# Optimization experiments

Hardware: AMD Instinct MI355X
Metric: run time of the kernel (lower is better)

## Reference

```python
import jax, jax.numpy as jnp
import numpy as np

DIM = 256
NUM_HEADS = 4
HEAD_DIM = DIM // NUM_HEADS
SCALE = HEAD_DIM ** -0.5


def setup_inputs() -> dict:
    key = jax.random.key(0)
    ks = jax.random.split(key, 11)
    B, Nq, Nkv = 4, 2048, 2048
    inp = {
        "query_feat": jax.random.normal(ks[0], (B, Nq, DIM), dtype=jnp.float32),
        "key_value_feat": jax.random.normal(ks[1], (B, Nkv, DIM), dtype=jnp.float32),
        "reliability_kv": jax.random.uniform(ks[2], (B, Nkv), dtype=jnp.float32),
        "Wq": jax.random.normal(ks[3], (DIM, DIM), dtype=jnp.float32) * (DIM ** -0.5),
        "bq": jnp.zeros((DIM,), jnp.float32),
        "Wk": jax.random.normal(ks[4], (DIM, DIM), dtype=jnp.float32) * (DIM ** -0.5),
        "bk": jnp.zeros((DIM,), jnp.float32),
        "Wv": jax.random.normal(ks[5], (DIM, DIM), dtype=jnp.float32) * (DIM ** -0.5),
        "bv": jnp.zeros((DIM,), jnp.float32),
        "Wo": jax.random.normal(ks[6], (DIM, DIM), dtype=jnp.float32) * (DIM ** -0.5),
        "bo": jnp.zeros((DIM,), jnp.float32),
    }
    return inp


def _heads(x):
    B, N, C = x.shape
    return x.reshape(B, N, NUM_HEADS, HEAD_DIM).transpose(0, 2, 1, 3)  # [B,H,N,hd]


def reference(query_feat, key_value_feat, reliability_kv, Wq, bq, Wk, bk, Wv, bv, Wo, bo):
    B, Nq, _ = query_feat.shape
    q = _heads(query_feat @ Wq + bq)          # [B,H,Nq,hd]
    k = _heads(key_value_feat @ Wk + bk)      # [B,H,Nkv,hd]
    v = _heads(key_value_feat @ Wv + bv)
    # gate K/V by reliability (broadcast over heads and head_dim)
    rk = reliability_kv[:, None, :, None]     # [B,1,Nkv,1]
    k = k * rk
    v = v * rk
    attn = jnp.einsum("bhqd,bhkd->bhqk", q, k) * SCALE
    log_r = jnp.log(jnp.clip(reliability_kv, 1e-6))[:, None, None, :]  # [B,1,1,Nkv]
    attn = jax.nn.softmax(attn + log_r, axis=-1)  # [B,H,Nq,Nkv]
    out = jnp.einsum("bhqk,bhkd->bhqd", attn, v)
    out = out.transpose(0, 2, 1, 3).reshape(B, Nq, DIM)
    out = out @ Wo + bo
    attn_mean = attn.mean(axis=1)  # [B,Nq,Nkv]
    return out, attn_mean
```

## Files before the change

### kernel.cpp

```cpp
#include <hip/hip_runtime.h>


typedef __attribute__((ext_vector_type(8))) _Float16 half8;
typedef __attribute__((ext_vector_type(4))) _Float16 half4;
typedef __attribute__((ext_vector_type(2))) __fp16 fp16x2;
typedef __attribute__((ext_vector_type(4))) float f32x4;

#define MFMAH32(A, B, C) __builtin_amdgcn_mfma_f32_16x16x32_f16((A), (B), (C), 0, 0, 0)
#define MFMAH16(A, B, C) __builtin_amdgcn_mfma_f32_16x16x16f16((A), (B), (C), 0, 0, 0)

__device__ __forceinline__ unsigned short f2h(float f) {
    union { _Float16 h; unsigned short u; } c; c.h = (_Float16)f; return c.u;
}
__device__ __forceinline__ float h2f(unsigned short u) {
    union { unsigned short u; _Float16 h; } c; c.u = u; return (float)c.h;
}
__device__ __forceinline__ half8 ldh8(const unsigned short* p) {
    return *reinterpret_cast<const half8*>(p);
}
__device__ __forceinline__ half4 ldh4(const unsigned short* p) {
    return *reinterpret_cast<const half4*>(p);
}
__device__ __forceinline__ half4 pk4(float a, float b, float c, float d) {
    union { fp16x2 h2[2]; half4 h4; } u;
    u.h2[0] = __builtin_amdgcn_cvt_pkrtz(a, b);
    u.h2[1] = __builtin_amdgcn_cvt_pkrtz(c, d);
    return u.h4;
}
__device__ __forceinline__ void gld16(const unsigned short* g, unsigned short* l) {
    __builtin_amdgcn_global_load_lds(
        (const __attribute__((address_space(1))) unsigned int*)g,
        (__attribute__((address_space(3))) unsigned int*)l, 16, 0, 0);
}

__global__ void wsplit_kernel(const float* __restrict__ Wq, const float* __restrict__ Wk,
                              const float* __restrict__ Wv, const float* __restrict__ Wo,
                              unsigned short* __restrict__ WT) {
    int e = blockIdx.x * 256 + threadIdx.x;
    int m = e >> 16;
    int idx = e & 65535;
    int k = idx >> 8, n = idx & 255;
    const float* W = (m == 0) ? Wq : (m == 1) ? Wk : (m == 2) ? Wv : Wo;
    WT[m * 65536 + n * 256 + k] = f2h(W[idx]);
}

#define STAGE_W(dst_, src_, kt_) do {                                               \
    _Pragma("unroll")                                                               \
    for (int j_ = 0; j_ < 4; ++j_) {                                                \
        int s_ = w * 4 + j_;                                                        \
        int rowl_ = 8 * s_ + (l >> 3);                                              \
        int so_ = rowl_ * 256 + (kt_) * 64 + (((l & 7) ^ (rowl_ & 7)) << 3);        \
        gld16(&(src_)[so_], &(dst_)[s_ * 512]);                                     \
    }                                                                               \
} while (0)

#define GEMM_TILE(buf_, kt_) do {                                                   \
    _Pragma("unroll")                                                               \
    for (int ksl_ = 0; ksl_ < 2; ++ksl_) {                                          \
        _Pragma("unroll")                                                           \
        for (int n_ = 0; n_ < 16; ++n_) {                                           \
            int r_ = n_ * 16 + l15;                                                 \
            int idx_ = r_ * 64 + ((((ksl_)*4 + lg) ^ (r_ & 7)) << 3);               \
            half8 b_ = ldh8(&(buf_)[idx_]);                                         \
            acc[n_] = MFMAH32(ah[(kt_) * 2 + ksl_], b_, acc[n_]);                   \
        }                                                                           \
    }                                                                               \
} while (0)

__global__ __launch_bounds__(512, 1) void proj3_kernel(
    const float* __restrict__ query, const float* __restrict__ kv,
    const float* __restrict__ rel, const unsigned short* __restrict__ WT,
    const float* __restrict__ bq, const float* __restrict__ bk, const float* __restrict__ bv,
    unsigned short* __restrict__ Qh, unsigned short* __restrict__ Kh,
    unsigned short* __restrict__ Vtmp) {
    const int job = blockIdx.y;
    const float* X = (job == 0) ? query : kv;
    const unsigned short* wg = WT + job * 65536;
    const float* bias = (job == 0) ? bq : (job == 1) ? bk : bv;
    const float* rs = (job == 0) ? nullptr : rel;
    unsigned short* oh = (job == 0) ? Qh : (job == 1) ? Kh : Vtmp;

    __shared__ __align__(16) unsigned short wlds[2][256 * 64];

    const int w = threadIdx.x >> 6, l = threadIdx.x & 63;
    const int l15 = l & 15, lg = l >> 4;
    const int arow = blockIdx.x * 128 + w * 16 + l15;

    half8 ah[8];
#pragma unroll
    for (int ks = 0; ks < 8; ++ks) {
        const float* p = &X[arow * 256 + ks * 32 + lg * 8];
        float4 f0 = *reinterpret_cast<const float4*>(p);
        float4 f1 = *reinterpret_cast<const float4*>(p + 4);
        half8 t;
        t[0] = (_Float16)f0.x; t[1] = (_Float16)f0.y; t[2] = (_Float16)f0.z; t[3] = (_Float16)f0.w;
        t[4] = (_Float16)f1.x; t[5] = (_Float16)f1.y; t[6] = (_Float16)f1.z; t[7] = (_Float16)f1.w;
        ah[ks] = t;
    }
    f32x4 acc[16];
#pragma unroll
    for (int n = 0; n < 16; ++n) acc[n] = (f32x4){0.f, 0.f, 0.f, 0.f};

    STAGE_W(wlds[0], wg, 0);
    __syncthreads();
#pragma unroll
    for (int kt = 0; kt < 4; ++kt) {
        const int cur = kt & 1, nx = cur ^ 1;
        if (kt < 3) STAGE_W(wlds[nx], wg, kt + 1);
        GEMM_TILE(wlds[cur], kt);
        __syncthreads();
    }

    const int orow0 = blockIdx.x * 128 + w * 16 + lg * 4;
    float rsv[4];
#pragma unroll
    for (int r = 0; r < 4; ++r) rsv[r] = rs ? rs[orow0 + r] : 1.0f;
#pragma unroll
    for (int n = 0; n < 16; ++n) {
        const int col = n * 16 + l15;
        const float bn = bias[col];
#pragma unroll
        for (int r = 0; r < 4; ++r)
            oh[(orow0 + r) * 256 + col] = f2h((acc[n][r] + bn) * rsv[r]);
    }
}

__global__ void transpose_v_kernel(const unsigned short* __restrict__ Vtmp,
                                   unsigned short* __restrict__ Vt) {
    __shared__ unsigned short tile[16][264];
    const int st = blockIdx.x, b = blockIdx.y;
    const int t = threadIdx.x;
#pragma unroll
    for (int it = 0; it < 4; ++it) {
        int idx = it * 256 + t;
        int kr = idx >> 6;
        int d4 = (idx & 63) * 4;
        ushort4 v = *reinterpret_cast<const ushort4*>(
            &Vtmp[(size_t)(b * 2048 + st * 16 + kr) * 256 + d4]);
        tile[kr][d4 + 0] = v.x; tile[kr][d4 + 1] = v.y;
        tile[kr][d4 + 2] = v.z; tile[kr][d4 + 3] = v.w;
    }
    __syncthreads();
    {
        const int d = t;
        unsigned int u[8];
#pragma unroll
        for (int k2 = 0; k2 < 8; ++k2)
            u[k2] = (unsigned int)tile[k2 * 2][d] | ((unsigned int)tile[k2 * 2 + 1][d] << 16);
        uint4* dst = reinterpret_cast<uint4*>(&Vt[((size_t)(b * 128 + st) * 256 + d) * 16]);
        dst[0] = (uint4){u[0], u[1], u[2], u[3]};
        dst[1] = (uint4){u[4], u[5], u[6], u[7]};
    }
}

__global__ __launch_bounds__(512, 2) void attn_pass1(
    const unsigned short* __restrict__ Qh, const unsigned short* __restrict__ Kh,
    const unsigned short* __restrict__ Vt, const float* __restrict__ rel,
    float* __restrict__ po_a, float* __restrict__ po_b, float* __restrict__ ps) {
    const int bid = blockIdx.x;
    const int sw = (bid & 7) * 32 + (bid >> 3);
    const int b = sw >> 6;
    const int rem = sw & 63;
    const int kh = rem & 1;
    const int q0 = (rem >> 1) * 64;
    const int tid = threadIdx.x;
    const int w = tid >> 6, h = w & 3, ks = w >> 2;
    const int l = tid & 63, l15 = l & 15, lg = l >> 4;
    const float C2 = 0.18033688011112042f;

    __shared__ __align__(16) unsigned short ldsKV[2][8][2][1024];
    __shared__ float rel_lr[2048];
    __shared__ float ssum_sh[2][4][64];

    {
        float4 v = reinterpret_cast<const float4*>(&rel[b * 2048])[tid];
        float* d = &rel_lr[tid * 4];
        d[0] = log2f(fmaxf(v.x, 1e-6f)); d[1] = log2f(fmaxf(v.y, 1e-6f));
        d[2] = log2f(fmaxf(v.z, 1e-6f)); d[3] = log2f(fmaxf(v.w, 1e-6f));
    }

    half8 qf[4][2];
#pragma unroll
    for (int qs = 0; qs < 4; ++qs)
#pragma unroll
        for (int kd = 0; kd < 2; ++kd)
            qf[qs][kd] = ldh8(&Qh[(b * 2048 + q0 + qs * 16 + l15) * 256 +
                                  h * 64 + kd * 32 + lg * 8]);
    __syncthreads();

    const int st0 = kh * 64 + ks * 32;

#define STG(buf_, i_) do {                                                          \
    const unsigned short* kbp_ = Kh + (size_t)(b * 2048 + (st0 + (i_)) * 16) * 256  \
                                 + h * 64;                                          \
    _Pragma("unroll")                                                               \
    for (int j_ = 0; j_ < 2; ++j_) {                                                \
        int r_ = j_ * 8 + (l >> 3);                                                 \
        gld16(kbp_ + r_ * 256 + (((l & 7) ^ ((l >> 3) & 7)) << 3),                  \
              &ldsKV[0][w][buf_][j_ * 512]);                                        \
    }                                                                               \
    const unsigned short* vbp_ = Vt + (size_t)((b * 128 + st0 + (i_)) * 256         \
                                 + h * 64) * 16;                                    \
    _Pragma("unroll")                                                               \
    for (int j_ = 0; j_ < 2; ++j_) {                                                \
        int d_ = j_ * 32 + (l >> 1);                                                \
        gld16(vbp_ + d_ * 16 + (((l & 1) ^ ((l >> 1) & 1)) << 3),                   \
              &ldsKV[1][w][buf_][j_ * 512]);                                        \
    }                                                                               \
} while (0)

    float ssum[4] = {0.f, 0.f, 0.f, 0.f};
    f32x4 oacc[4][4];
#pragma unroll
    for (int qs = 0; qs < 4; ++qs)
#pragma unroll
        for (int dc = 0; dc < 4; ++dc)
            oacc[qs][dc] = (f32x4){0.f, 0.f, 0.f, 0.f};

    STG(0, 0);
    for (int i = 0; i < 32; ++i) {
        const int cur = i & 1, nx = cur ^ 1;
        if (i < 31) {
            STG(nx, i + 1);
            asm volatile("s_waitcnt vmcnt(4)" ::: "memory");
        } else {
            asm volatile("s_waitcnt vmcnt(0)" ::: "memory");
        }
        __builtin_amdgcn_sched_barrier(0);
        half8 kf0 = ldh8(&ldsKV[0][w][cur][l15 * 64 + ((lg ^ (l15 & 7)) << 3)]);
        half8 kf1 = ldh8(&ldsKV[0][w][cur][l15 * 64 + (((4 + lg) ^ (l15 & 7)) << 3)]);
        f32x4 a[4];
#pragma unroll
        for (int qs = 0; qs < 4; ++qs) {
            f32x4 t = (f32x4){0.f, 0.f, 0.f, 0.f};
            t = MFMAH32(kf0, qf[qs][0], t);
            t = MFMAH32(kf1, qf[qs][1], t);
            a[qs] = t;
        }
        float4 lr4 = *reinterpret_cast<const float4*>(&rel_lr[(st0 + i) * 16 + lg * 4]);
        half4 pa[4];
#pragma unroll
        for (int qs = 0; qs < 4; ++qs) {
            float p0 = exp2f(__builtin_fmaf(a[qs][0], C2, lr4.x));
            float p1 = exp2f(__builtin_fmaf(a[qs][1], C2, lr4.y));
            float p2 = exp2f(__builtin_fmaf(a[qs][2], C2, lr4.z));
            float p3 = exp2f(__builtin_fmaf(a[qs][3], C2, lr4.w));
            ssum[qs] += (p0 + p1) + (p2 + p3);
            pa[qs] = pk4(p0, p1, p2, p3);
        }
#pragma unroll
        for (int dc = 0; dc < 4; ++dc) {
            const int d = dc * 16 + l15;
            half4 vf = ldh4(&ldsKV[1][w][cur][d * 16 +
                            ((((lg >> 1) ^ (d & 1))) << 3) + (lg & 1) * 4]);
#pragma unroll
            for (int qs = 0; qs < 4; ++qs)
                oacc[qs][dc] = MFMAH16(pa[qs], vf, oacc[qs][dc]);
        }
    }
#undef STG

    float vred[4];
#pragma unroll
    for (int qs = 0; qs < 4; ++qs) {
        float v = ssum[qs];
        v += __shfl_xor(v, 16); v += __shfl_xor(v, 32);
        vred[qs] = v;
    }

    __syncthreads();
    if (l < 16) {
#pragma unroll
        for (int qs = 0; qs < 4; ++qs)
            ssum_sh[ks][h][qs * 16 + l] = vred[qs];
    }
    float* obuf = (float*)&ldsKV[0][0][0][0];
    if (ks == 1) {
#pragma unroll
        for (int qs = 0; qs < 4; ++qs)
#pragma unroll
            for (int dc = 0; dc < 4; ++dc)
#pragma unroll
                for (int r = 0; r < 4; ++r)
                    obuf[(qs * 16 + lg * 4 + r) * 256 + h * 64 + dc * 16 + l15] =
                        oacc[qs][dc][r];
    }
    __syncthreads();
    if (ks == 0) {
        const int chunk = b * 2 + kh;
        float* po = (chunk < 2) ? (po_a + (size_t)chunk * 524288)
                                : (po_b + (size_t)(chunk - 2) * 524288);
#pragma unroll
        for (int qs = 0; qs < 4; ++qs)
#pragma unroll
            for (int dc = 0; dc < 4; ++dc)
#pragma unroll
                for (int r = 0; r < 4; ++r) {
                    const int d = h * 64 + dc * 16 + l15;
                    const int q = qs * 16 + lg * 4 + r;
                    po[(size_t)(q0 + q) * 256 + d] = oacc[qs][dc][r] + obuf[q * 256 + d];
                }
        if (l < 16) {
#pragma unroll
            for (int qs = 0; qs < 4; ++qs)
                ps[(chunk * 4 + h) * 2048 + q0 + qs * 16 + l] =
                    ssum_sh[0][h][qs * 16 + l] + ssum_sh[1][h][qs * 16 + l];
        }
    }
}

__global__ __launch_bounds__(256) void combine_kernel(
    const float* __restrict__ po_a, const float* __restrict__ po_b,
    const float* __restrict__ ps, unsigned short* __restrict__ AO,
    float* __restrict__ sinv_ws) {
    const int t = blockIdx.x * 256 + threadIdx.x;
    const int d4 = t & 63;
    const int bq = t >> 6;
    const int q = bq & 2047;
    const int b = bq >> 11;
    const int d0 = d4 * 4, h = d0 >> 6;
    const int c0 = b * 2, c1 = b * 2 + 1;
    const float* p0 = (c0 < 2) ? po_a + (size_t)c0 * 524288 : po_b + (size_t)(c0 - 2) * 524288;
    const float* p1 = (c1 < 2) ? po_a + (size_t)c1 * 524288 : po_b + (size_t)(c1 - 2) * 524288;
    float4 x = *reinterpret_cast<const float4*>(&p0[(size_t)q * 256 + d0]);
    float4 y = *reinterpret_cast<const float4*>(&p1[(size_t)q * 256 + d0]);
    float s = ps[(c0 * 4 + h) * 2048 + q] + ps[(c1 * 4 + h) * 2048 + q];
    float si = 1.0f / s;
    ushort4 o;
    o.x = f2h((x.x + y.x) * si); o.y = f2h((x.y + y.y) * si);
    o.z = f2h((x.z + y.z) * si); o.w = f2h((x.w + y.w) * si);
    *reinterpret_cast<ushort4*>(&AO[((size_t)(b * 2048 + q)) * 256 + d0]) = o;
    if (d4 == (h << 4)) sinv_ws[(b * 4 + h) * 2048 + q] = si;
}

__global__ __launch_bounds__(256, 4) void attn_mean_kernel(
    const unsigned short* __restrict__ Qh, const unsigned short* __restrict__ Kh,
    const float* __restrict__ rel, const float* __restrict__ sinv_ws,
    float* __restrict__ attn_mean) {
    const int kslice = blockIdx.x >> 7;
    const int inner = blockIdx.x & 127;
    const int sw = (inner & 7) * 16 + (inner >> 3);
    const int b = sw >> 5;
    const int q0 = (sw & 31) * 64;
    const int tid = threadIdx.x;
    const int w = tid >> 6;
    const int l = tid & 63, l15 = l & 15, lg = l >> 4;
    const int kb = b * 2048;
    const float C2 = 0.18033688011112042f;

    __shared__ __align__(16) unsigned short ldsK[2][8192];
    __shared__ float rel_lr[2048];

#define STAGE_KM(dst_, kt_) do {                                                    \
    _Pragma("unroll")                                                               \
    for (int j_ = 0; j_ < 4; ++j_) {                                                \
        int s_ = w * 4 + j_;                                                        \
        int r_ = 2 * s_ + (l >> 5);                                                 \
        size_t so_ = (size_t)(kb + (kt_) * 32 + r_) * 256 +                         \
                     (((l & 31) ^ (r_ & 7)) << 3);                                  \
        gld16(&Kh[so_], &(dst_)[s_ * 512]);                                         \
    }                                                                               \
} while (0)

    {
        float4 v0 = reinterpret_cast<const float4*>(&rel[b * 2048])[tid * 2];
        float4 v1 = reinterpret_cast<const float4*>(&rel[b * 2048])[tid * 2 + 1];
        float* d = &rel_lr[tid * 8];
        d[0] = log2f(fmaxf(v0.x, 1e-6f)); d[1] = log2f(fmaxf(v0.y, 1e-6f));
        d[2] = log2f(fmaxf(v0.z, 1e-6f)); d[3] = log2f(fmaxf(v0.w, 1e-6f));
        d[4] = log2f(fmaxf(v1.x, 1e-6f)); d[5] = log2f(fmaxf(v1.y, 1e-6f));
        d[6] = log2f(fmaxf(v1.z, 1e-6f)); d[7] = log2f(fmaxf(v1.w, 1e-6f));
    }

    half8 qf[4][2];
    {
        const int qrow = b * 2048 + q0 + w * 16 + l15;
#pragma unroll
        for (int h = 0; h < 4; ++h)
#pragma unroll
            for (int kd = 0; kd < 2; ++kd)
                qf[h][kd] = ldh8(&Qh[qrow * 256 + h * 64 + kd * 32 + lg * 8]);
    }
    float lsi[4][4];
#pragma unroll
    for (int h = 0; h < 4; ++h)
#pragma unroll
        for (int r4 = 0; r4 < 4; ++r4)
            lsi[h][r4] = log2f(sinv_ws[(b * 4 + h) * 2048 + q0 + w * 16 + lg * 4 + r4]) - 2.0f;
    __syncthreads();

    const int kt0 = kslice * 8;
    STAGE_KM(ldsK[0], kt0);
    for (int ki = 0; ki < 8; ++ki) {
        const int kt = kt0 + ki;
        const int cur = ki & 1, nx = cur ^ 1;
        if (ki < 7) {
            STAGE_KM(ldsK[nx], kt + 1);
            asm volatile("s_waitcnt vmcnt(4)" ::: "memory");
        } else {
            asm volatile("s_waitcnt vmcnt(0)" ::: "memory");
        }
        asm volatile("s_barrier" ::: "memory");
        __builtin_amdgcn_sched_barrier(0);
#pragma unroll
        for (int kc = 0; kc < 2; ++kc) {
            const int r = kc * 16 + l15;
            const int rx = r & 7;
            f32x4 a[4];
#pragma unroll
            for (int h = 0; h < 4; ++h) {
                half8 kf0 = ldh8(&ldsK[cur][r * 256 + (((h * 8 + lg) ^ rx) << 3)]);
                half8 kf1 = ldh8(&ldsK[cur][r * 256 + (((h * 8 + 4 + lg) ^ rx) << 3)]);
                f32x4 t = (f32x4){0.f, 0.f, 0.f, 0.f};
                t = MFMAH32(qf[h][0], kf0, t);
                t = MFMAH32(qf[h][1], kf1, t);
                a[h] = t;
            }
            const float lr = rel_lr[kt * 32 + kc * 16 + l15];
            const size_t kcol = (size_t)(kt * 32 + kc * 16 + l15);
#pragma unroll
            for (int r4 = 0; r4 < 4; ++r4) {
                float m = exp2f(__builtin_fmaf(a[0][r4], C2, lsi[0][r4]) + lr)
                        + exp2f(__builtin_fmaf(a[1][r4], C2, lsi[1][r4]) + lr)
                        + exp2f(__builtin_fmaf(a[2][r4], C2, lsi[2][r4]) + lr)
                        + exp2f(__builtin_fmaf(a[3][r4], C2, lsi[3][r4]) + lr);
                attn_mean[(size_t)(b * 2048 + q0 + w * 16 + lg * 4 + r4) * 2048 + kcol] = m;
            }
        }
        asm volatile("s_waitcnt lgkmcnt(0)\n\ts_barrier" ::: "memory");
    }
#undef STAGE_KM
}

__global__ __launch_bounds__(512, 1) void final_kernel(
    const unsigned short* __restrict__ AO, const unsigned short* __restrict__ WoT,
    const float* __restrict__ bo, float* __restrict__ out) {
    __shared__ __align__(16) unsigned short wlds[2][256 * 64];

    const int w = threadIdx.x >> 6, l = threadIdx.x & 63;
    const int l15 = l & 15, lg = l >> 4;
    const int arow = blockIdx.x * 128 + w * 16 + l15;

    half8 ah[8];
#pragma unroll
    for (int ks = 0; ks < 8; ++ks)
        ah[ks] = ldh8(&AO[arow * 256 + ks * 32 + lg * 8]);
    f32x4 acc[16];
#pragma unroll
    for (int n = 0; n < 16; ++n) acc[n] = (f32x4){0.f, 0.f, 0.f, 0.f};

    STAGE_W(wlds[0], WoT, 0);
    __syncthreads();
#pragma unroll
    for (int kt = 0; kt < 4; ++kt) {
        const int cur = kt & 1, nx = cur ^ 1;
        if (kt < 3) STAGE_W(wlds[nx], WoT, kt + 1);
        GEMM_TILE(wlds[cur], kt);
        __syncthreads();
    }

    const int orow0 = blockIdx.x * 128 + w * 16 + lg * 4;
#pragma unroll
    for (int n = 0; n < 16; ++n) {
        const int col = n * 16 + l15;
        const float bn = bo[col];
#pragma unroll
        for (int r = 0; r < 4; ++r)
            out[(orow0 + r) * 256 + col] = acc[n][r] + bn;
    }
}

extern "C" void kernel_launch(void* const* d_in, const int* in_sizes, int n_in,
                              void* d_out, int out_size, void* d_ws, size_t ws_size,
                              hipStream_t stream) {
    const float* query = (const float*)d_in[0];
    const float* kv    = (const float*)d_in[1];
    const float* rel   = (const float*)d_in[2];
    const float* Wq    = (const float*)d_in[3];
    const float* bq    = (const float*)d_in[4];
    const float* Wk    = (const float*)d_in[5];
    const float* bk    = (const float*)d_in[6];
    const float* Wv    = (const float*)d_in[7];
    const float* bv    = (const float*)d_in[8];
    const float* Wo    = (const float*)d_in[9];
    const float* bo    = (const float*)d_in[10];

    char* ws = (char*)d_ws;
    unsigned short* WT   = (unsigned short*)(ws + 0);
    unsigned short* Qh   = (unsigned short*)(ws + 524288);
    unsigned short* Kh   = (unsigned short*)(ws + 4718592);
    unsigned short* Vtmp = (unsigned short*)(ws + 8912896);
    unsigned short* Vt   = (unsigned short*)(ws + 13107200);
    unsigned short* AO   = (unsigned short*)(ws + 17301504);
    float*          sinv = (float*)(ws + 21495808);
    float*          ps   = (float*)(ws + 21626880);
    float*          po_b = (float*)(ws + 21889024);
    float*          po_a = (float*)Vtmp;

    float* out = (float*)d_out;
    float* attn_mean = (float*)d_out + 2097152;

    wsplit_kernel<<<1024, 256, 0, stream>>>(Wq, Wk, Wv, Wo, WT);
    proj3_kernel<<<dim3(64, 3), 512, 0, stream>>>(query, kv, rel, WT,
                                                  bq, bk, bv, Qh, Kh, Vtmp);
    transpose_v_kernel<<<dim3(128, 4), 256, 0, stream>>>(Vtmp, Vt);
    attn_pass1<<<256, 512, 0, stream>>>(Qh, Kh, Vt, rel, po_a, po_b, ps);
    combine_kernel<<<2048, 256, 0, stream>>>(po_a, po_b, ps, AO, sinv);
    attn_mean_kernel<<<1024, 256, 0, stream>>>(Qh, Kh, rel, sinv, attn_mean);
    final_kernel<<<64, 512, 0, stream>>>(AO, WT + 3 * 65536, bo, out);
}
```

Measured before the change: 109.8 us.

## Re-split attention pass into smaller blocks with one q-tile per wave

The first attention pass now launches 1024 blocks of 256 threads instead of 256 blocks of 512. Each block handles 16 queries, and each wave covers one head over a full 64-tile key half. This removes the intra-block split-K reduction through LDS and its barriers, and raises the block count to fill more CUs. The cost is four times more K/V traffic per query, since each K/V tile now feeds only one 16-row query tile. Both the attention pass and the attn_mean kernel also precompute their global load base offsets once and advance them by a running offset, which cuts per-iteration address arithmetic.

```diff
diff --git a/kernel.cpp b/kernel.cpp
--- a/kernel.cpp
+++ b/kernel.cpp
@@ -153,160 +153,120 @@
     }
 }
 
-__global__ __launch_bounds__(512, 2) void attn_pass1(
+__global__ __launch_bounds__(256, 4) void attn_pass1(
     const unsigned short* __restrict__ Qh, const unsigned short* __restrict__ Kh,
     const unsigned short* __restrict__ Vt, const float* __restrict__ rel,
     float* __restrict__ po_a, float* __restrict__ po_b, float* __restrict__ ps) {
     const int bid = blockIdx.x;
-    const int sw = (bid & 7) * 32 + (bid >> 3);
-    const int b = sw >> 6;
-    const int rem = sw & 63;
+    const int sw = (bid & 7) * 128 + (bid >> 3);
+    const int b = sw >> 8;
+    const int rem = sw & 255;
     const int kh = rem & 1;
-    const int q0 = (rem >> 1) * 64;
+    const int q0 = (rem >> 1) * 16;
     const int tid = threadIdx.x;
-    const int w = tid >> 6, h = w & 3, ks = w >> 2;
+    const int w = tid >> 6, h = w;
     const int l = tid & 63, l15 = l & 15, lg = l >> 4;
     const float C2 = 0.18033688011112042f;
 
-    __shared__ __align__(16) unsigned short ldsKV[2][8][2][1024];
+    __shared__ __align__(16) unsigned short ldsKV[2][4][2][1024];
     __shared__ float rel_lr[2048];
-    __shared__ float ssum_sh[2][4][64];
-
-    {
-        float4 v = reinterpret_cast<const float4*>(&rel[b * 2048])[tid];
-        float* d = &rel_lr[tid * 4];
-        d[0] = log2f(fmaxf(v.x, 1e-6f)); d[1] = log2f(fmaxf(v.y, 1e-6f));
-        d[2] = log2f(fmaxf(v.z, 1e-6f)); d[3] = log2f(fmaxf(v.w, 1e-6f));
-    }
-
-    half8 qf[4][2];
-#pragma unroll
-    for (int qs = 0; qs < 4; ++qs)
-#pragma unroll
-        for (int kd = 0; kd < 2; ++kd)
-            qf[qs][kd] = ldh8(&Qh[(b * 2048 + q0 + qs * 16 + l15) * 256 +
-                                  h * 64 + kd * 32 + lg * 8]);
+
+    {
+        float4 v0 = reinterpret_cast<const float4*>(&rel[b * 2048])[tid * 2];
+        float4 v1 = reinterpret_cast<const float4*>(&rel[b * 2048])[tid * 2 + 1];
+        float* d = &rel_lr[tid * 8];
+        d[0] = log2f(fmaxf(v0.x, 1e-6f)); d[1] = log2f(fmaxf(v0.y, 1e-6f));
+        d[2] = log2f(fmaxf(v0.z, 1e-6f)); d[3] = log2f(fmaxf(v0.w, 1e-6f));
+        d[4] = log2f(fmaxf(v1.x, 1e-6f)); d[5] = log2f(fmaxf(v1.y, 1e-6f));
+        d[6] = log2f(fmaxf(v1.z, 1e-6f)); d[7] = log2f(fmaxf(v1.w, 1e-6f));
+    }
+
+    half8 qf0, qf1;
+    {
+        const int o0 = (b * 2048 + q0 + l15) * 256 + h * 64 + lg * 8;
+        qf0 = ldh8(&Qh[o0]); qf1 = ldh8(&Qh[o0 + 32]);
+    }
     __syncthreads();
 
-    const int st0 = kh * 64 + ks * 32;
-
-#define STG(buf_, i_) do {                                                          \
-    const unsigned short* kbp_ = Kh + (size_t)(b * 2048 + (st0 + (i_)) * 16) * 256  \
-                                 + h * 64;                                          \
-    _Pragma("unroll")                                                               \
-    for (int j_ = 0; j_ < 2; ++j_) {                                                \
-        int r_ = j_ * 8 + (l >> 3);                                                 \
-        gld16(kbp_ + r_ * 256 + (((l & 7) ^ ((l >> 3) & 7)) << 3),                  \
-              &ldsKV[0][w][buf_][j_ * 512]);                                        \
-    }                                                                               \
-    const unsigned short* vbp_ = Vt + (size_t)((b * 128 + st0 + (i_)) * 256         \
-                                 + h * 64) * 16;                                    \
-    _Pragma("unroll")                                                               \
-    for (int j_ = 0; j_ < 2; ++j_) {                                                \
-        int d_ = j_ * 32 + (l >> 1);                                                \
-        gld16(vbp_ + d_ * 16 + (((l & 1) ^ ((l >> 1) & 1)) << 3),                   \
-              &ldsKV[1][w][buf_][j_ * 512]);                                        \
-    }                                                                               \
+    const int st0 = kh * 64;
+
+    size_t kb_[2], vb_[2];
+    {
+        const int swzK = ((l & 7) ^ ((l >> 3) & 7)) << 3;
+        const int swzV = ((l & 1) ^ ((l >> 1) & 1)) << 3;
+#pragma unroll
+        for (int j = 0; j < 2; ++j) {
+            int kr = j * 8 + (l >> 3);
+            kb_[j] = (size_t)(b * 2048 + st0 * 16 + kr) * 256 + h * 64 + swzK;
+            int vd = j * 32 + (l >> 1);
+            vb_[j] = (size_t)((b * 128 + st0) * 256 + h * 64 + vd) * 16 + swzV;
+        }
+    }
+    unsigned short* myK = &ldsKV[0][w][0][0];
+    unsigned short* myV = &ldsKV[1][w][0][0];
+    const int kOff0 = l15 * 64 + ((lg ^ (l15 & 7)) << 3);
+    const int kOff1 = l15 * 64 + (((4 + lg) ^ (l15 & 7)) << 3);
+    int vOff[4];
+#pragma unroll
+    for (int dc = 0; dc < 4; ++dc)
+        vOff[dc] = (dc * 16 + l15) * 16 + (((lg >> 1) ^ (l15 & 1)) << 3) + (lg & 1) * 4;
+
+#define STG2(buf_, off_) do {                                                       \
+    gld16(&Kh[kb_[0] + (off_)], &myK[(buf_) * 1024]);                               \
+    gld16(&Kh[kb_[1] + (off_)], &myK[(buf_) * 1024 + 512]);                         \
+    gld16(&Vt[vb_[0] + (off_)], &myV[(buf_) * 1024]);                               \
+    gld16(&Vt[vb_[1] + (off_)], &myV[(buf_) * 1024 + 512]);                         \
 } while (0)
 
-    float ssum[4] = {0.f, 0.f, 0.f, 0.f};
-    f32x4 oacc[4][4];
-#pragma unroll
-    for (int qs = 0; qs < 4; ++qs)
-#pragma unroll
-        for (int dc = 0; dc < 4; ++dc)
-            oacc[qs][dc] = (f32x4){0.f, 0.f, 0.f, 0.f};
-
-    STG(0, 0);
-    for (int i = 0; i < 32; ++i) {
+    float ssum = 0.f;
+    f32x4 oacc[4];
+#pragma unroll
+    for (int dc = 0; dc < 4; ++dc) oacc[dc] = (f32x4){0.f, 0.f, 0.f, 0.f};
+
+    STG2(0, 0);
+    size_t offn = 4096;
+    for (int i = 0; i < 64; ++i) {
         const int cur = i & 1, nx = cur ^ 1;
-        if (i < 31) {
-            STG(nx, i + 1);
+        if (i < 63) {
+            STG2(nx, offn); offn += 4096;
             asm volatile("s_waitcnt vmcnt(4)" ::: "memory");
         } else {
             asm volatile("s_waitcnt vmcnt(0)" ::: "memory");
         }
         __builtin_amdgcn_sched_barrier(0);
-        half8 kf0 = ldh8(&ldsKV[0][w][cur][l15 * 64 + ((lg ^ (l15 & 7)) << 3)]);
-        half8 kf1 = ldh8(&ldsKV[0][w][cur][l15 * 64 + (((4 + lg) ^ (l15 & 7)) << 3)]);
-        f32x4 a[4];
-#pragma unroll
-        for (int qs = 0; qs < 4; ++qs) {
-            f32x4 t = (f32x4){0.f, 0.f, 0.f, 0.f};
-            t = MFMAH32(kf0, qf[qs][0], t);
-            t = MFMAH32(kf1, qf[qs][1], t);
-            a[qs] = t;
-        }
+        half8 kf0 = ldh8(&myK[cur * 1024 + kOff0]);
+        half8 kf1 = ldh8(&myK[cur * 1024 + kOff1]);
+        f32x4 a = (f32x4){0.f, 0.f, 0.f, 0.f};
+        a = MFMAH32(kf0, qf0, a);
+        a = MFMAH32(kf1, qf1, a);
         float4 lr4 = *reinterpret_cast<const float4*>(&rel_lr[(st0 + i) * 16 + lg * 4]);
-        half4 pa[4];
-#pragma unroll
-        for (int qs = 0; qs < 4; ++qs) {
-            float p0 = exp2f(__builtin_fmaf(a[qs][0], C2, lr4.x));
-            float p1 = exp2f(__builtin_fmaf(a[qs][1], C2, lr4.y));
-            float p2 = exp2f(__builtin_fmaf(a[qs][2], C2, lr4.z));
-            float p3 = exp2f(__builtin_fmaf(a[qs][3], C2, lr4.w));
-            ssum[qs] += (p0 + p1) + (p2 + p3);
-            pa[qs] = pk4(p0, p1, p2, p3);
-        }
+        float p0 = exp2f(__builtin_fmaf(a[0], C2, lr4.x));
+        float p1 = exp2f(__builtin_fmaf(a[1], C2, lr4.y));
+        float p2 = exp2f(__builtin_fmaf(a[2], C2, lr4.z));
+        float p3 = exp2f(__builtin_fmaf(a[3], C2, lr4.w));
+        ssum += (p0 + p1) + (p2 + p3);
+        half4 pa = pk4(p0, p1, p2, p3);
 #pragma unroll
         for (int dc = 0; dc < 4; ++dc) {
-            const int d = dc * 16 + l15;
-            half4 vf = ldh4(&ldsKV[1][w][cur][d * 16 +
-                            ((((lg >> 1) ^ (d & 1))) << 3) + (lg & 1) * 4]);
-#pragma unroll
-            for (int qs = 0; qs < 4; ++qs)
-                oacc[qs][dc] = MFMAH16(pa[qs], vf, oacc[qs][dc]);
-        }
-    }
-#undef STG
-
-    float vred[4];
-#pragma unroll
-    for (int qs = 0; qs < 4; ++qs) {
-        float v = ssum[qs];
-        v += __shfl_xor(v, 16); v += __shfl_xor(v, 32);
-        vred[qs] = v;
-    }
-
-    __syncthreads();
-    if (l < 16) {
-#pragma unroll
-        for (int qs = 0; qs < 4; ++qs)
-            ssum_sh[ks][h][qs * 16 + l] = vred[qs];
-    }
-    float* obuf = (float*)&ldsKV[0][0][0][0];
-    if (ks == 1) {
-#pragma unroll
-        for (int qs = 0; qs < 4; ++qs)
-#pragma unroll
-            for (int dc = 0; dc < 4; ++dc)
-#pragma unroll
-                for (int r = 0; r < 4; ++r)
-                    obuf[(qs * 16 + lg * 4 + r) * 256 + h * 64 + dc * 16 + l15] =
-                        oacc[qs][dc][r];
-    }
-    __syncthreads();
-    if (ks == 0) {
-        const int chunk = b * 2 + kh;
-        float* po = (chunk < 2) ? (po_a + (size_t)chunk * 524288)
-                                : (po_b + (size_t)(chunk - 2) * 524288);
-#pragma unroll
-        for (int qs = 0; qs < 4; ++qs)
-#pragma unroll
-            for (int dc = 0; dc < 4; ++dc)
-#pragma unroll
-                for (int r = 0; r < 4; ++r) {
-                    const int d = h * 64 + dc * 16 + l15;
-                    const int q = qs * 16 + lg * 4 + r;
-                    po[(size_t)(q0 + q) * 256 + d] = oacc[qs][dc][r] + obuf[q * 256 + d];
-                }
-        if (l < 16) {
-#pragma unroll
-            for (int qs = 0; qs < 4; ++qs)
-                ps[(chunk * 4 + h) * 2048 + q0 + qs * 16 + l] =
-                    ssum_sh[0][h][qs * 16 + l] + ssum_sh[1][h][qs * 16 + l];
-        }
-    }
+            half4 vf = ldh4(&myV[cur * 1024 + vOff[dc]]);
+            oacc[dc] = MFMAH16(pa, vf, oacc[dc]);
+        }
+    }
+#undef STG2
+
+    float v = ssum;
+    v += __shfl_xor(v, 16); v += __shfl_xor(v, 32);
+
+    const int chunk = b * 2 + kh;
+    float* po = (chunk < 2) ? (po_a + (size_t)chunk * 524288)
+                            : (po_b + (size_t)(chunk - 2) * 524288);
+#pragma unroll
+    for (int dc = 0; dc < 4; ++dc)
+#pragma unroll
+        for (int r = 0; r < 4; ++r)
+            po[(size_t)(q0 + lg * 4 + r) * 256 + h * 64 + dc * 16 + l15] = oacc[dc][r];
+    if (l < 16)
+        ps[(chunk * 4 + h) * 2048 + q0 + l] = v;
 }
 
 __global__ __launch_bounds__(256) void combine_kernel(
@@ -351,17 +311,6 @@
     __shared__ __align__(16) unsigned short ldsK[2][8192];
     __shared__ float rel_lr[2048];
 
-#define STAGE_KM(dst_, kt_) do {                                                    \
-    _Pragma("unroll")                                                               \
-    for (int j_ = 0; j_ < 4; ++j_) {                                                \
-        int s_ = w * 4 + j_;                                                        \
-        int r_ = 2 * s_ + (l >> 5);                                                 \
-        size_t so_ = (size_t)(kb + (kt_) * 32 + r_) * 256 +                         \
-                     (((l & 31) ^ (r_ & 7)) << 3);                                  \
-        gld16(&Kh[so_], &(dst_)[s_ * 512]);                                         \
-    }                                                                               \
-} while (0)
-
     {
         float4 v0 = reinterpret_cast<const float4*>(&rel[b * 2048])[tid * 2];
         float4 v1 = reinterpret_cast<const float4*>(&rel[b * 2048])[tid * 2 + 1];
@@ -387,15 +336,34 @@
 #pragma unroll
         for (int r4 = 0; r4 < 4; ++r4)
             lsi[h][r4] = log2f(sinv_ws[(b * 4 + h) * 2048 + q0 + w * 16 + lg * 4 + r4]) - 2.0f;
+
+    size_t kmb[4];
+    {
+#pragma unroll
+        for (int j = 0; j < 4; ++j) {
+            int s_ = w * 4 + j;
+            int r_ = 2 * s_ + (l >> 5);
+            kmb[j] = (size_t)(kb + r_) * 256 + (((l & 31) ^ (r_ & 7)) << 3);
+        }
+    }
+#define STAGE_KM2(dst_, off_) do {                                                  \
+    gld16(&Kh[kmb[0] + (off_)], &(dst_)[(w * 4 + 0) * 512]);                        \
+    gld16(&Kh[kmb[1] + (off_)], &(dst_)[(w * 4 + 1) * 512]);                        \
+    gld16(&Kh[kmb[2] + (off_)], &(dst_)[(w * 4 + 2) * 512]);                        \
+    gld16(&Kh[kmb[3] + (off_)], &(dst_)[(w * 4 + 3) * 512]);                        \
+} while (0)
+
     __syncthreads();
 
     const int kt0 = kslice * 8;
-    STAGE_KM(ldsK[0], kt0);
+    size_t moff = (size_t)kt0 * 8192;
+    STAGE_KM2(ldsK[0], moff);
     for (int ki = 0; ki < 8; ++ki) {
         const int kt = kt0 + ki;
         const int cur = ki & 1, nx = cur ^ 1;
         if (ki < 7) {
-            STAGE_KM(ldsK[nx], kt + 1);
+            STAGE_KM2(ldsK[nx], moff + 8192);
+            moff += 8192;
             asm volatile("s_waitcnt vmcnt(4)" ::: "memory");
         } else {
             asm volatile("s_waitcnt vmcnt(0)" ::: "memory");
@@ -429,7 +397,7 @@
         }
         asm volatile("s_waitcnt lgkmcnt(0)\n\ts_barrier" ::: "memory");
     }
-#undef STAGE_KM
+#undef STAGE_KM2
 }
 
 __global__ __launch_bounds__(512, 1) void final_kernel(
@@ -504,7 +472,7 @@
     proj3_kernel<<<dim3(64, 3), 512, 0, stream>>>(query, kv, rel, WT,
                                                   bq, bk, bv, Qh, Kh, Vtmp);
     transpose_v_kernel<<<dim3(128, 4), 256, 0, stream>>>(Vtmp, Vt);
-    attn_pass1<<<256, 512, 0, stream>>>(Qh, Kh, Vt, rel, po_a, po_b, ps);
+    attn_pass1<<<1024, 256, 0, stream>>>(Qh, Kh, Vt, rel, po_a, po_b, ps);
     combine_kernel<<<2048, 256, 0, stream>>>(po_a, po_b, ps, AO, sinv);
     attn_mean_kernel<<<1024, 256, 0, stream>>>(Qh, Kh, rel, sinv, attn_mean);
     final_kernel<<<64, 512, 0, stream>>>(AO, WT + 3 * 65536, bo, out);
```

Result: slower. 115.9 us (+5.6%).
